# Kernel tuning notes

Measured on AMD Instinct MI355X. Metric: run time of the kernel, lower is better.

The kernel has to match this reference:

```python
import jax, jax.numpy as jnp
import numpy as np

D = 64          # slot_dim == input_dim
K = 8           # num_slots
NUM_ITERS = 3
EPS = 1e-8      # attention renorm eps
LN_EPS = 1e-5   # torch LayerNorm default
SCALE = float(np.sqrt(D))


def _ln(x, g, b):
    m = x.mean(-1, keepdims=True)
    v = ((x - m) ** 2).mean(-1, keepdims=True)
    return (x - m) / jnp.sqrt(v + LN_EPS) * g + b


def setup_inputs() -> dict:
    key = jax.random.key(0)
    ks = jax.random.split(key, 12)
    B, N = 128, 4096
    s = 1.0 / np.sqrt(D)
    return {
        "inputs": jax.random.normal(ks[0], (B, N, D), jnp.float32),
        "noise": jax.random.normal(ks[1], (B, K, D), jnp.float32),
        "slot_mu": jax.random.normal(ks[2], (1, 1, D), jnp.float32),
        "slot_log_sigma": jnp.zeros((1, 1, D), jnp.float32),
        "Wq": jax.random.normal(ks[3], (D, D), jnp.float32) * s,
        "Wk": jax.random.normal(ks[4], (D, D), jnp.float32) * s,
        "Wv": jax.random.normal(ks[5], (D, D), jnp.float32) * s,
        "gru_wih": jax.random.normal(ks[6], (3 * D, D), jnp.float32) * s,
        "gru_whh": jax.random.normal(ks[7], (3 * D, D), jnp.float32) * s,
        "gru_bih": jnp.zeros((3 * D,), jnp.float32),
        "gru_bhh": jnp.zeros((3 * D,), jnp.float32),
        "ln_in_g": jnp.ones((D,), jnp.float32),
        "ln_in_b": jnp.zeros((D,), jnp.float32),
        "ln_s_g": jnp.ones((D,), jnp.float32),
        "ln_s_b": jnp.zeros((D,), jnp.float32),
        "mlp_ln_g": jnp.ones((D,), jnp.float32),
        "mlp_ln_b": jnp.zeros((D,), jnp.float32),
        "mlp_w1": jax.random.normal(ks[8], (4 * D, D), jnp.float32) * s,
        "mlp_b1": jnp.zeros((4 * D,), jnp.float32),
        "mlp_w2": jax.random.normal(ks[9], (D, 4 * D), jnp.float32) * (1.0 / np.sqrt(4 * D)),
        "mlp_b2": jnp.zeros((D,), jnp.float32),
    }


def reference(inputs, noise, slot_mu, slot_log_sigma, Wq, Wk, Wv,
              gru_wih, gru_whh, gru_bih, gru_bhh,
              ln_in_g, ln_in_b, ln_s_g, ln_s_b,
              mlp_ln_g, mlp_ln_b, mlp_w1, mlp_b1, mlp_w2, mlp_b2):
    x = _ln(inputs, ln_in_g, ln_in_b)          # (B, N, D)
    k = x @ Wk.T                               # (B, N, D)
    v = x @ Wv.T                               # (B, N, D)
    slots = slot_mu + jnp.exp(slot_log_sigma) * noise  # (B, K, D)
    for _ in range(NUM_ITERS):
        slots_prev = slots
        s = _ln(slots, ln_s_g, ln_s_b)
        q = s @ Wq.T                           # (B, K, D)
        attn = jnp.einsum('bkd,bnd->bkn', q, k) / SCALE
        attn = jax.nn.softmax(attn, axis=1)    # compete over slots
        attn_w = attn / (attn.sum(-1, keepdims=True) + EPS)
        updates = jnp.einsum('bkn,bnd->bkd', attn_w, v)
        # GRUCell(updates, slots_prev)
        gi = updates @ gru_wih.T + gru_bih
        gh = slots_prev @ gru_whh.T + gru_bhh
        i_r, i_z, i_n = jnp.split(gi, 3, axis=-1)
        h_r, h_z, h_n = jnp.split(gh, 3, axis=-1)
        r = jax.nn.sigmoid(i_r + h_r)
        z = jax.nn.sigmoid(i_z + h_z)
        n = jnp.tanh(i_n + r * h_n)
        slots = (1.0 - z) * n + z * slots_prev
        # residual MLP
        h = _ln(slots, mlp_ln_g, mlp_ln_b)
        slots = slots + jax.nn.relu(h @ mlp_w1.T + mlp_b1) @ mlp_w2.T + mlp_b2
    return slots
```

## Files before the change

kernel.cpp:

```cpp
#include <hip/hip_runtime.h>
#include <cstdint>

#define Bn 128
#define Nn 4096
#define Dn 64
#define Kn 8
#define PBn 8
#define NCHUNKn (Nn / PBn)
#define LN_EPSf 1e-5f
#define EPSf 1e-8f

typedef unsigned short u16x8 __attribute__((ext_vector_type(8)));

static __device__ __forceinline__ uint16_t f2bf(float f) {
    union { float f; uint32_t u; } v; v.f = f;
    return (uint16_t)((v.u + 0x7fffu + ((v.u >> 16) & 1u)) >> 16);
}
static __device__ __forceinline__ float bflo(uint32_t u) {
    union { uint32_t u; float f; } v; v.u = u << 16; return v.f;
}
static __device__ __forceinline__ float bfhi(uint32_t u) {
    union { uint32_t u; float f; } v; v.u = u & 0xffff0000u; return v.f;
}

template <int CTRL>
static __device__ __forceinline__ float dppadd(float x) {
    int p = __builtin_amdgcn_update_dpp(0, __float_as_int(x), CTRL, 0xf, 0xf, false);
    return x + __int_as_float(p);
}

__global__ __launch_bounds__(256) void kinit(const float* __restrict__ noise,
                                             const float* __restrict__ mu,
                                             const float* __restrict__ ls,
                                             float* __restrict__ slots) {
    int i = blockIdx.x * 256 + threadIdx.x;
    int base = i * 4;
    int d = base & 63;
    float4 nz = *(const float4*)(noise + base);
    float4 m  = *(const float4*)(mu + d);
    float4 s  = *(const float4*)(ls + d);
    float4 o;
    o.x = m.x + __expf(s.x) * nz.x;
    o.y = m.y + __expf(s.y) * nz.y;
    o.z = m.z + __expf(s.z) * nz.z;
    o.w = m.w + __expf(s.w) * nz.w;
    *(float4*)(slots + base) = o;
}

__global__ __launch_bounds__(256) void kM(const float* __restrict__ Wq,
                                          const float* __restrict__ Wk,
                                          float* __restrict__ M) {
    const int idx = blockIdx.x * 256 + threadIdx.x;
    const int e = idx >> 6, f = idx & 63;
    float acc = 0.f;
#pragma unroll 8
    for (int d = 0; d < 64; ++d) acc += Wq[d * 64 + e] * Wk[d * 64 + f];
    M[idx] = acc * 0.125f;
}

__global__ __launch_bounds__(256) void k1_ln(const float* __restrict__ inp,
                                             const float* __restrict__ lng,
                                             const float* __restrict__ lnb,
                                             uint16_t* __restrict__ xout) {
    const int t = threadIdx.x;
    const long row = (long)blockIdx.x * 64 + (t >> 2);
    const int c0 = (t & 3) * 16;

    const float* src = inp + row * 64 + c0;
    float x[16];
#pragma unroll
    for (int u = 0; u < 4; ++u) {
        float4 v4 = *(const float4*)(src + u * 4);
        x[u * 4 + 0] = v4.x; x[u * 4 + 1] = v4.y;
        x[u * 4 + 2] = v4.z; x[u * 4 + 3] = v4.w;
    }
    float s1 = 0.f, s2 = 0.f;
#pragma unroll
    for (int i = 0; i < 16; ++i) { s1 += x[i]; s2 += x[i] * x[i]; }
    s1 = dppadd<0xB1>(s1); s2 = dppadd<0xB1>(s2);
    s1 = dppadd<0x4E>(s1); s2 = dppadd<0x4E>(s2);
    const float mean = s1 * (1.0f / 64.0f);
    const float var = s2 * (1.0f / 64.0f) - mean * mean;
    const float rstd = rsqrtf(var + LN_EPSf);

    u16x8 o0, o1;
#pragma unroll
    for (int i = 0; i < 8; ++i) {
        o0[i] = f2bf((x[i] - mean) * rstd * lng[c0 + i] + lnb[c0 + i]);
        o1[i] = f2bf((x[8 + i] - mean) * rstd * lng[c0 + 8 + i] + lnb[c0 + 8 + i]);
    }
    uint16_t* dst = xout + row * 64 + c0;
    *(u16x8*)dst = o0;
    *(u16x8*)(dst + 8) = o1;
}

__global__ __launch_bounds__(256) void k2_attn(
    const uint16_t* __restrict__ xbf, const float* __restrict__ slots,
    const float* __restrict__ M, const float* __restrict__ lsg,
    const float* __restrict__ lsb, float* __restrict__ partials) {
    __shared__ float sraw[Kn * Dn];
    __shared__ float sln[Kn][68];
    __shared__ float qld[Kn][64];
    __shared__ float red[16 * 552];
    __shared__ float redas[16][8];

    const int t = threadIdx.x;
    const int b = blockIdx.x >> 3;
    const int part = blockIdx.x & 7;

    if (t < 128) *(float4*)(sraw + t * 4) = *(const float4*)(slots + b * 512 + t * 4);
    __syncthreads();

    if (t < 128) {
        const int row = t >> 4, l16 = t & 15;
        float4 v4 = *(const float4*)(sraw + row * 64 + l16 * 4);
        float s1 = v4.x + v4.y + v4.z + v4.w;
        float s2 = v4.x * v4.x + v4.y * v4.y + v4.z * v4.z + v4.w * v4.w;
        s1 = dppadd<0xB1>(s1); s2 = dppadd<0xB1>(s2);
        s1 = dppadd<0x4E>(s1); s2 = dppadd<0x4E>(s2);
        s1 = dppadd<0x141>(s1); s2 = dppadd<0x141>(s2);
        s1 = dppadd<0x128>(s1); s2 = dppadd<0x128>(s2);
        const float mean = s1 * (1.0f / 64.0f);
        const float var = s2 * (1.0f / 64.0f) - mean * mean;
        const float rstd = rsqrtf(var + LN_EPSf);
        const float xs[4] = {v4.x, v4.y, v4.z, v4.w};
#pragma unroll
        for (int i = 0; i < 4; ++i) {
            const int dcol = l16 * 4 + i;
            sln[row][dcol] = (xs[i] - mean) * rstd * lsg[dcol] + lsb[dcol];
        }
    }
    __syncthreads();

    {
        const int kk0 = t >> 6, kk1 = kk0 + 4;
        const int j = t & 63;
        float a0 = 0.f, a1 = 0.f;
#pragma unroll 8
        for (int e = 0; e < 64; ++e) {
            const float m = M[e * 64 + j];
            a0 += sln[kk0][e] * m;
            a1 += sln[kk1][e] * m;
        }
        qld[kk0][j] = a0;
        qld[kk1][j] = a1;
    }
    __syncthreads();

    const int dc = t & 7;
    const int pg = t >> 3;
    float qr[8][8];
#pragma unroll
    for (int kk = 0; kk < 8; ++kk) {
        float4 q0 = *(const float4*)&qld[kk][dc * 8];
        float4 q1 = *(const float4*)&qld[kk][dc * 8 + 4];
        qr[kk][0] = q0.x; qr[kk][1] = q0.y; qr[kk][2] = q0.z; qr[kk][3] = q0.w;
        qr[kk][4] = q1.x; qr[kk][5] = q1.y; qr[kk][6] = q1.z; qr[kk][7] = q1.w;
    }

    float upd[8][8];
    float asum[8];
#pragma unroll
    for (int kk = 0; kk < 8; ++kk) {
        asum[kk] = 0.f;
#pragma unroll
        for (int i = 0; i < 8; ++i) upd[kk][i] = 0.f;
    }

    const uint16_t* xbase = xbf + ((long)b * Nn + part * NCHUNKn) * 64 + dc * 8;

    uint4 xr = *(const uint4*)(xbase + (long)pg * 64);

    for (int it = 0; it < NCHUNKn / 32; ++it) {
        uint4 xn = xr;
        if (it < NCHUNKn / 32 - 1)
            xn = *(const uint4*)(xbase + (long)((it + 1) * 32 + pg) * 64);
        float xf[8];
        xf[0] = bflo(xr.x); xf[1] = bfhi(xr.x);
        xf[2] = bflo(xr.y); xf[3] = bfhi(xr.y);
        xf[4] = bflo(xr.z); xf[5] = bfhi(xr.z);
        xf[6] = bflo(xr.w); xf[7] = bfhi(xr.w);

        float lg[8];
#pragma unroll
        for (int kk = 0; kk < 8; ++kk) {
            float a = 0.f;
#pragma unroll
            for (int i = 0; i < 8; ++i) a += qr[kk][i] * xf[i];
            lg[kk] = a;
        }
#pragma unroll
        for (int kk = 0; kk < 8; ++kk) lg[kk] = dppadd<0xB1>(lg[kk]);
#pragma unroll
        for (int kk = 0; kk < 8; ++kk) lg[kk] = dppadd<0x4E>(lg[kk]);
#pragma unroll
        for (int kk = 0; kk < 8; ++kk) lg[kk] = dppadd<0x141>(lg[kk]);
        float mx = lg[0];
#pragma unroll
        for (int kk = 1; kk < 8; ++kk) mx = fmaxf(mx, lg[kk]);
        float e[8];
        float es = 0.f;
#pragma unroll
        for (int kk = 0; kk < 8; ++kk) { e[kk] = __expf(lg[kk] - mx); es += e[kk]; }
        const float rinv = 1.0f / es;
#pragma unroll
        for (int kk = 0; kk < 8; ++kk) {
            const float a = e[kk] * rinv;
            asum[kk] += a;
#pragma unroll
            for (int i = 0; i < 8; ++i) upd[kk][i] += a * xf[i];
        }
        xr = xn;
    }

#pragma unroll
    for (int kk = 0; kk < 8; ++kk) {
#pragma unroll
        for (int i = 0; i < 8; ++i) upd[kk][i] = dppadd<0x128>(upd[kk][i]);
        asum[kk] = dppadd<0x128>(asum[kk]);
    }
    const int l = t & 63;
    const int wv = t >> 6;
    if ((l & 8) == 0) {
        const int copy = wv * 4 + (l >> 4);
        float* rb = red + copy * 552 + (l & 7) * 8;
#pragma unroll
        for (int kk = 0; kk < 8; ++kk) {
            float4 u0, u1;
            u0.x = upd[kk][0]; u0.y = upd[kk][1]; u0.z = upd[kk][2]; u0.w = upd[kk][3];
            u1.x = upd[kk][4]; u1.y = upd[kk][5]; u1.z = upd[kk][6]; u1.w = upd[kk][7];
            *(float4*)(rb + kk * 68) = u0;
            *(float4*)(rb + kk * 68 + 4) = u1;
        }
        if ((l & 15) == 0) {
            float4 a0, a1;
            a0.x = asum[0]; a0.y = asum[1]; a0.z = asum[2]; a0.w = asum[3];
            a1.x = asum[4]; a1.y = asum[5]; a1.z = asum[6]; a1.w = asum[7];
            *(float4*)&redas[copy][0] = a0;
            *(float4*)&redas[copy][4] = a1;
        }
    }
    __syncthreads();
    float* pout = partials + (long)(b * PBn + part) * 520;
    if (t < 128) {
        const int kk = t >> 4, dq = t & 15;
        float4 acc = {0.f, 0.f, 0.f, 0.f};
#pragma unroll
        for (int c = 0; c < 16; ++c) {
            float4 v = *(const float4*)(red + c * 552 + kk * 68 + dq * 4);
            acc.x += v.x; acc.y += v.y; acc.z += v.z; acc.w += v.w;
        }
        *(float4*)(pout + kk * 64 + dq * 4) = acc;
    }
    if (t < 8) {
        float a = 0.f;
#pragma unroll
        for (int c = 0; c < 16; ++c) a += redas[c][t];
        pout[512 + t] = a;
    }
}

__global__ __launch_bounds__(256) void k3_update(
    const float* __restrict__ partials, const float* __restrict__ slots_in,
    const float* __restrict__ Wv,
    const float* __restrict__ wih, const float* __restrict__ whh,
    const float* __restrict__ bih, const float* __restrict__ bhh,
    const float* __restrict__ mg, const float* __restrict__ mb,
    const float* __restrict__ w1, const float* __restrict__ b1,
    const float* __restrict__ w2, const float* __restrict__ b2,
    float* __restrict__ slots_out) {
    __shared__ float axn[64];
    __shared__ float updf[64];
    __shared__ float sp[64];
    __shared__ float gi[192];
    __shared__ float gh[192];
    __shared__ float sn[64];
    __shared__ float hln[64];
    __shared__ float hid[256];

    const int t = threadIdx.x;
    const int b = blockIdx.x >> 3;
    const int s = blockIdx.x & 7;
    const float* pp = partials + (long)b * PBn * 520;

    float asum = EPSf;
#pragma unroll
    for (int j = 0; j < PBn; ++j) asum += pp[j * 520 + 512 + s];
    const float rasum = 1.0f / asum;

    if (t < 64) {
        float a = 0.f;
#pragma unroll
        for (int j = 0; j < PBn; ++j) a += pp[j * 520 + s * 64 + t];
        axn[t] = a * rasum;
    } else if (t < 80) {
        const int i = t - 64;
        *(float4*)&sp[i * 4] = *(const float4*)(slots_in + b * 512 + s * 64 + i * 4);
    }
    __syncthreads();

    {
        const int d = t >> 2, h = t & 3;
        const float* wr = Wv + d * 64 + h * 16;
        float acc = 0.f;
#pragma unroll
        for (int u = 0; u < 4; ++u) {
            float4 w4 = *(const float4*)(wr + u * 4);
            float4 a4 = *(const float4*)&axn[h * 16 + u * 4];
            acc += w4.x * a4.x + w4.y * a4.y + w4.z * a4.z + w4.w * a4.w;
        }
        acc = dppadd<0xB1>(acc);
        acc = dppadd<0x4E>(acc);
        if (h == 0) updf[d] = acc;
    }
    __syncthreads();

    for (int w = t; w < 768; w += 256) {
        const int j = w >> 2, h = w & 3;
        const float* wr = wih + j * 64 + h * 16;
        float acc = 0.f;
#pragma unroll
        for (int u = 0; u < 4; ++u) {
            float4 w4 = *(const float4*)(wr + u * 4);
            float4 a4 = *(const float4*)&updf[h * 16 + u * 4];
            acc += w4.x * a4.x + w4.y * a4.y + w4.z * a4.z + w4.w * a4.w;
        }
        acc = dppadd<0xB1>(acc);
        acc = dppadd<0x4E>(acc);
        if (h == 0) gi[j] = acc + bih[j];
    }
    for (int w = t; w < 768; w += 256) {
        const int j = w >> 2, h = w & 3;
        const float* wr = whh + j * 64 + h * 16;
        float acc = 0.f;
#pragma unroll
        for (int u = 0; u < 4; ++u) {
            float4 w4 = *(const float4*)(wr + u * 4);
            float4 a4 = *(const float4*)&sp[h * 16 + u * 4];
            acc += w4.x * a4.x + w4.y * a4.y + w4.z * a4.z + w4.w * a4.w;
        }
        acc = dppadd<0xB1>(acc);
        acc = dppadd<0x4E>(acc);
        if (h == 0) gh[j] = acc + bhh[j];
    }
    __syncthreads();

    if (t < 64) {
        const float ir = gi[t], iz = gi[64 + t], in_ = gi[128 + t];
        const float hr = gh[t], hz = gh[64 + t], hn = gh[128 + t];
        const float r = 1.0f / (1.0f + __expf(-(ir + hr)));
        const float z = 1.0f / (1.0f + __expf(-(iz + hz)));
        const float n = tanhf(in_ + r * hn);
        sn[t] = (1.0f - z) * n + z * sp[t];
    }
    __syncthreads();

    if (t < 16) {
        float4 v4 = *(const float4*)&sn[t * 4];
        float s1 = v4.x + v4.y + v4.z + v4.w;
        float s2 = v4.x * v4.x + v4.y * v4.y + v4.z * v4.z + v4.w * v4.w;
        s1 = dppadd<0xB1>(s1); s2 = dppadd<0xB1>(s2);
        s1 = dppadd<0x4E>(s1); s2 = dppadd<0x4E>(s2);
        s1 = dppadd<0x141>(s1); s2 = dppadd<0x141>(s2);
        s1 = dppadd<0x128>(s1); s2 = dppadd<0x128>(s2);
        const float mean = s1 * (1.0f / 64.0f);
        const float var = s2 * (1.0f / 64.0f) - mean * mean;
        const float rstd = rsqrtf(var + LN_EPSf);
        const float xs[4] = {v4.x, v4.y, v4.z, v4.w};
#pragma unroll
        for (int i = 0; i < 4; ++i) {
            const int dcol = t * 4 + i;
            hln[dcol] = (xs[i] - mean) * rstd * mg[dcol] + mb[dcol];
        }
    }
    __syncthreads();

    for (int w = t; w < 1024; w += 256) {
        const int j = w >> 2, h = w & 3;
        const float* wr = w1 + j * 64 + h * 16;
        float acc = 0.f;
#pragma unroll
        for (int u = 0; u < 4; ++u) {
            float4 w4 = *(const float4*)(wr + u * 4);
            float4 a4 = *(const float4*)&hln[h * 16 + u * 4];
            acc += w4.x * a4.x + w4.y * a4.y + w4.z * a4.z + w4.w * a4.w;
        }
        acc = dppadd<0xB1>(acc);
        acc = dppadd<0x4E>(acc);
        if (h == 0) hid[j] = fmaxf(acc + b1[j], 0.0f);
    }
    __syncthreads();

    {
        const int d = t >> 2, h = t & 3;
        const float* wr = w2 + d * 256 + h * 64;
        float acc = 0.f;
#pragma unroll
        for (int u = 0; u < 16; ++u) {
            float4 w4 = *(const float4*)(wr + u * 4);
            float4 h4 = *(const float4*)&hid[h * 64 + u * 4];
            acc += w4.x * h4.x + w4.y * h4.y + w4.z * h4.z + w4.w * h4.w;
        }
        acc = dppadd<0xB1>(acc);
        acc = dppadd<0x4E>(acc);
        if (h == 0) slots_out[(long)b * 512 + s * 64 + d] = sn[d] + acc + b2[d];
    }
}

extern "C" void kernel_launch(void* const* d_in, const int* in_sizes, int n_in,
                              void* d_out, int out_size, void* d_ws, size_t ws_size,
                              hipStream_t stream) {
    const float* inputs = (const float*)d_in[0];
    const float* noise = (const float*)d_in[1];
    const float* mu = (const float*)d_in[2];
    const float* ls = (const float*)d_in[3];
    const float* Wq = (const float*)d_in[4];
    const float* Wk = (const float*)d_in[5];
    const float* Wv = (const float*)d_in[6];
    const float* wih = (const float*)d_in[7];
    const float* whh = (const float*)d_in[8];
    const float* bih = (const float*)d_in[9];
    const float* bhh = (const float*)d_in[10];
    const float* lng = (const float*)d_in[11];
    const float* lnb = (const float*)d_in[12];
    const float* lsg = (const float*)d_in[13];
    const float* lsb = (const float*)d_in[14];
    const float* mg = (const float*)d_in[15];
    const float* mb = (const float*)d_in[16];
    const float* w1 = (const float*)d_in[17];
    const float* b1 = (const float*)d_in[18];
    const float* w2 = (const float*)d_in[19];
    const float* b2 = (const float*)d_in[20];

    char* ws = (char*)d_ws;
    float* slots = (float*)ws;
    float* Mm = (float*)(ws + 262144);
    uint16_t* xbf = (uint16_t*)(ws + 262144 + 16384);
    float* parts = (float*)(ws + 262144 + 16384 + (1 << 26));

    kinit<<<64, 256, 0, stream>>>(noise, mu, ls, slots);
    kM<<<16, 256, 0, stream>>>(Wq, Wk, Mm);
    k1_ln<<<8192, 256, 0, stream>>>(inputs, lng, lnb, xbf);
    for (int it = 0; it < 3; ++it) {
        k2_attn<<<Bn * PBn, 256, 0, stream>>>(xbf, slots, Mm, lsg, lsb, parts);
        float* dst = (it == 2) ? (float*)d_out : slots;
        k3_update<<<Bn * Kn, 256, 0, stream>>>(parts, slots, Wv, wih, whh, bih, bhh,
                                               mg, mb, w1, b1, w2, b2, dst);
    }
}
```

Baseline: 210.4 us.

## Split attention over more blocks and process two tokens per loop iteration

Each batch's token range is now split across 16 blocks instead of 8, which doubles the grid of the attention kernel to raise occupancy. The inner loop is fully unrolled and handles two tokens per iteration with two outstanding loads, adding instruction-level parallelism. The softmax across slots no longer subtracts the running maximum, and it uses a hardware reciprocal instead of a divide, cutting ALU work per token. Dropping the max subtraction risks exp overflow if logits grow large. The larger split also doubles the partial buffers that the later reduction has to combine.

```diff
diff --git a/kernel.cpp b/kernel.cpp
--- a/kernel.cpp
+++ b/kernel.cpp
@@ -5,7 +5,7 @@
 #define Nn 4096
 #define Dn 64
 #define Kn 8
-#define PBn 8
+#define PBn 16
 #define NCHUNKn (Nn / PBn)
 #define LN_EPSf 1e-5f
 #define EPSf 1e-8f
@@ -105,8 +105,8 @@
     __shared__ float redas[16][8];
 
     const int t = threadIdx.x;
-    const int b = blockIdx.x >> 3;
-    const int part = blockIdx.x & 7;
+    const int b = blockIdx.x >> 4;
+    const int part = blockIdx.x & 15;
 
     if (t < 128) *(float4*)(sraw + t * 4) = *(const float4*)(slots + b * 512 + t * 4);
     __syncthreads();
@@ -169,48 +169,63 @@
 
     const uint16_t* xbase = xbf + ((long)b * Nn + part * NCHUNKn) * 64 + dc * 8;
 
-    uint4 xr = *(const uint4*)(xbase + (long)pg * 64);
-
-    for (int it = 0; it < NCHUNKn / 32; ++it) {
-        uint4 xn = xr;
-        if (it < NCHUNKn / 32 - 1)
-            xn = *(const uint4*)(xbase + (long)((it + 1) * 32 + pg) * 64);
-        float xf[8];
-        xf[0] = bflo(xr.x); xf[1] = bfhi(xr.x);
-        xf[2] = bflo(xr.y); xf[3] = bfhi(xr.y);
-        xf[4] = bflo(xr.z); xf[5] = bfhi(xr.z);
-        xf[6] = bflo(xr.w); xf[7] = bfhi(xr.w);
-
-        float lg[8];
+    uint4 xr0 = *(const uint4*)(xbase + (long)pg * 64);
+    uint4 xr1 = *(const uint4*)(xbase + (long)(32 + pg) * 64);
+
+#pragma unroll
+    for (int it = 0; it < NCHUNKn / 64; ++it) {
+        uint4 xn0 = xr0, xn1 = xr1;
+        if (it < NCHUNKn / 64 - 1) {
+            xn0 = *(const uint4*)(xbase + (long)((it + 1) * 64 + pg) * 64);
+            xn1 = *(const uint4*)(xbase + (long)((it + 1) * 64 + 32 + pg) * 64);
+        }
+        float xf0[8], xf1[8];
+        xf0[0] = bflo(xr0.x); xf0[1] = bfhi(xr0.x);
+        xf0[2] = bflo(xr0.y); xf0[3] = bfhi(xr0.y);
+        xf0[4] = bflo(xr0.z); xf0[5] = bfhi(xr0.z);
+        xf0[6] = bflo(xr0.w); xf0[7] = bfhi(xr0.w);
+        xf1[0] = bflo(xr1.x); xf1[1] = bfhi(xr1.x);
+        xf1[2] = bflo(xr1.y); xf1[3] = bfhi(xr1.y);
+        xf1[4] = bflo(xr1.z); xf1[5] = bfhi(xr1.z);
+        xf1[6] = bflo(xr1.w); xf1[7] = bfhi(xr1.w);
+
+        float lg0[8], lg1[8];
 #pragma unroll
         for (int kk = 0; kk < 8; ++kk) {
-            float a = 0.f;
-#pragma unroll
-            for (int i = 0; i < 8; ++i) a += qr[kk][i] * xf[i];
-            lg[kk] = a;
-        }
-#pragma unroll
-        for (int kk = 0; kk < 8; ++kk) lg[kk] = dppadd<0xB1>(lg[kk]);
-#pragma unroll
-        for (int kk = 0; kk < 8; ++kk) lg[kk] = dppadd<0x4E>(lg[kk]);
-#pragma unroll
-        for (int kk = 0; kk < 8; ++kk) lg[kk] = dppadd<0x141>(lg[kk]);
-        float mx = lg[0];
-#pragma unroll
-        for (int kk = 1; kk < 8; ++kk) mx = fmaxf(mx, lg[kk]);
-        float e[8];
-        float es = 0.f;
-#pragma unroll
-        for (int kk = 0; kk < 8; ++kk) { e[kk] = __expf(lg[kk] - mx); es += e[kk]; }
-        const float rinv = 1.0f / es;
+            float a0 = 0.f, a1 = 0.f;
+#pragma unroll
+            for (int i = 0; i < 8; ++i) {
+                a0 += qr[kk][i] * xf0[i];
+                a1 += qr[kk][i] * xf1[i];
+            }
+            lg0[kk] = a0;
+            lg1[kk] = a1;
+        }
+#pragma unroll
+        for (int kk = 0; kk < 8; ++kk) { lg0[kk] = dppadd<0xB1>(lg0[kk]); lg1[kk] = dppadd<0xB1>(lg1[kk]); }
+#pragma unroll
+        for (int kk = 0; kk < 8; ++kk) { lg0[kk] = dppadd<0x4E>(lg0[kk]); lg1[kk] = dppadd<0x4E>(lg1[kk]); }
+#pragma unroll
+        for (int kk = 0; kk < 8; ++kk) { lg0[kk] = dppadd<0x141>(lg0[kk]); lg1[kk] = dppadd<0x141>(lg1[kk]); }
+        float e0[8], e1[8];
+        float es0 = 0.f, es1 = 0.f;
 #pragma unroll
         for (int kk = 0; kk < 8; ++kk) {
-            const float a = e[kk] * rinv;
-            asum[kk] += a;
-#pragma unroll
-            for (int i = 0; i < 8; ++i) upd[kk][i] += a * xf[i];
-        }
-        xr = xn;
+            e0[kk] = __expf(lg0[kk]); es0 += e0[kk];
+            e1[kk] = __expf(lg1[kk]); es1 += e1[kk];
+        }
+        const float r0 = __builtin_amdgcn_rcpf(es0);
+        const float r1 = __builtin_amdgcn_rcpf(es1);
+#pragma unroll
+        for (int kk = 0; kk < 8; ++kk) {
+            const float a0 = e0[kk] * r0;
+            const float a1 = e1[kk] * r1;
+            asum[kk] += a0 + a1;
+#pragma unroll
+            for (int i = 0; i < 8; ++i)
+                upd[kk][i] += a0 * xf0[i] + a1 * xf1[i];
+        }
+        xr0 = xn0; xr1 = xn1;
     }
 
 #pragma unroll
```

Measured after the change: 282.7 us. 1.34x slower.

## Precompute slot queries in update kernel and simplify attention softmax with exp2

Applied to the files above, without the earlier changes.

Slot LayerNorm and the query projection through M are moved out of the attention kernel. They now run in an init kernel and at the end of the GRU/MLP update kernel, which writes a qk buffer. The attention kernel then only loads precomputed queries, so its 8 blocks per batch no longer each redo that work. The softmax over slots drops the max subtraction, uses exp2 with log2(e) folded into M, and uses a fast reciprocal. This trades numerical safety against overflow for fewer instructions per token. An unused kinit_qk kernel is left behind as dead code.

```diff
diff --git a/kernel.cpp b/kernel.cpp
--- a/kernel.cpp
+++ b/kernel.cpp
@@ -9,6 +9,7 @@
 #define NCHUNKn (Nn / PBn)
 #define LN_EPSf 1e-5f
 #define EPSf 1e-8f
+#define LOG2Ef 1.4426950408889634f
 
 typedef unsigned short u16x8 __attribute__((ext_vector_type(8)));
 
@@ -27,24 +28,6 @@
 static __device__ __forceinline__ float dppadd(float x) {
     int p = __builtin_amdgcn_update_dpp(0, __float_as_int(x), CTRL, 0xf, 0xf, false);
     return x + __int_as_float(p);
-}
-
-__global__ __launch_bounds__(256) void kinit(const float* __restrict__ noise,
-                                             const float* __restrict__ mu,
-                                             const float* __restrict__ ls,
-                                             float* __restrict__ slots) {
-    int i = blockIdx.x * 256 + threadIdx.x;
-    int base = i * 4;
-    int d = base & 63;
-    float4 nz = *(const float4*)(noise + base);
-    float4 m  = *(const float4*)(mu + d);
-    float4 s  = *(const float4*)(ls + d);
-    float4 o;
-    o.x = m.x + __expf(s.x) * nz.x;
-    o.y = m.y + __expf(s.y) * nz.y;
-    o.z = m.z + __expf(s.z) * nz.z;
-    o.w = m.w + __expf(s.w) * nz.w;
-    *(float4*)(slots + base) = o;
 }
 
 __global__ __launch_bounds__(256) void kM(const float* __restrict__ Wq,
@@ -55,62 +38,33 @@
     float acc = 0.f;
 #pragma unroll 8
     for (int d = 0; d < 64; ++d) acc += Wq[d * 64 + e] * Wk[d * 64 + f];
-    M[idx] = acc * 0.125f;
-}
-
-__global__ __launch_bounds__(256) void k1_ln(const float* __restrict__ inp,
-                                             const float* __restrict__ lng,
-                                             const float* __restrict__ lnb,
-                                             uint16_t* __restrict__ xout) {
-    const int t = threadIdx.x;
-    const long row = (long)blockIdx.x * 64 + (t >> 2);
-    const int c0 = (t & 3) * 16;
-
-    const float* src = inp + row * 64 + c0;
-    float x[16];
-#pragma unroll
-    for (int u = 0; u < 4; ++u) {
-        float4 v4 = *(const float4*)(src + u * 4);
-        x[u * 4 + 0] = v4.x; x[u * 4 + 1] = v4.y;
-        x[u * 4 + 2] = v4.z; x[u * 4 + 3] = v4.w;
-    }
-    float s1 = 0.f, s2 = 0.f;
-#pragma unroll
-    for (int i = 0; i < 16; ++i) { s1 += x[i]; s2 += x[i] * x[i]; }
-    s1 = dppadd<0xB1>(s1); s2 = dppadd<0xB1>(s2);
-    s1 = dppadd<0x4E>(s1); s2 = dppadd<0x4E>(s2);
-    const float mean = s1 * (1.0f / 64.0f);
-    const float var = s2 * (1.0f / 64.0f) - mean * mean;
-    const float rstd = rsqrtf(var + LN_EPSf);
-
-    u16x8 o0, o1;
-#pragma unroll
-    for (int i = 0; i < 8; ++i) {
-        o0[i] = f2bf((x[i] - mean) * rstd * lng[c0 + i] + lnb[c0 + i]);
-        o1[i] = f2bf((x[8 + i] - mean) * rstd * lng[c0 + 8 + i] + lnb[c0 + 8 + i]);
-    }
-    uint16_t* dst = xout + row * 64 + c0;
-    *(u16x8*)dst = o0;
-    *(u16x8*)(dst + 8) = o1;
-}
-
-__global__ __launch_bounds__(256) void k2_attn(
-    const uint16_t* __restrict__ xbf, const float* __restrict__ slots,
-    const float* __restrict__ M, const float* __restrict__ lsg,
-    const float* __restrict__ lsb, float* __restrict__ partials) {
+    M[idx] = acc * 0.125f * LOG2Ef;
+}
+
+__global__ __launch_bounds__(256) void kinit_qk(
+    const float* __restrict__ noise, const float* __restrict__ mu,
+    const float* __restrict__ ls, const float* __restrict__ M,
+    float* __restrict__ slots, float* __restrict__ qk) {
     __shared__ float sraw[Kn * Dn];
     __shared__ float sln[Kn][68];
-    __shared__ float qld[Kn][64];
-    __shared__ float red[16 * 552];
-    __shared__ float redas[16][8];
-
     const int t = threadIdx.x;
-    const int b = blockIdx.x >> 3;
-    const int part = blockIdx.x & 7;
-
-    if (t < 128) *(float4*)(sraw + t * 4) = *(const float4*)(slots + b * 512 + t * 4);
-    __syncthreads();
-
+    const int b = blockIdx.x;
+
+    if (t < 128) {
+        const int base = (b * 128 + t) * 4;
+        const int d = base & 63;
+        float4 nz = *(const float4*)(noise + base);
+        float4 m4 = *(const float4*)(mu + d);
+        float4 s4 = *(const float4*)(ls + d);
+        float4 o;
+        o.x = m4.x + __expf(s4.x) * nz.x;
+        o.y = m4.y + __expf(s4.y) * nz.y;
+        o.z = m4.z + __expf(s4.z) * nz.z;
+        o.w = m4.w + __expf(s4.w) * nz.w;
+        *(float4*)(slots + base) = o;
+        *(float4*)(sraw + t * 4) = o;
+    }
+    __syncthreads();
     if (t < 128) {
         const int row = t >> 4, l16 = t & 15;
         float4 v4 = *(const float4*)(sraw + row * 64 + l16 * 4);
@@ -125,26 +79,114 @@
         const float rstd = rsqrtf(var + LN_EPSf);
         const float xs[4] = {v4.x, v4.y, v4.z, v4.w};
 #pragma unroll
+        for (int i = 0; i < 4; ++i) sln[row][l16 * 4 + i] = (xs[i] - mean) * rstd;
+    }
+    __syncthreads();
+    ((void)0);
+}
+
+__global__ __launch_bounds__(256) void kinit_qk_full(
+    const float* __restrict__ noise, const float* __restrict__ mu,
+    const float* __restrict__ ls, const float* __restrict__ M,
+    const float* __restrict__ lsg, const float* __restrict__ lsb,
+    float* __restrict__ slots, float* __restrict__ qk) {
+    __shared__ float sraw[Kn * Dn];
+    __shared__ float sln[Kn][68];
+    const int t = threadIdx.x;
+    const int b = blockIdx.x;
+
+    if (t < 128) {
+        const int base = (b * 128 + t) * 4;
+        const int d = base & 63;
+        float4 nz = *(const float4*)(noise + base);
+        float4 m4 = *(const float4*)(mu + d);
+        float4 s4 = *(const float4*)(ls + d);
+        float4 o;
+        o.x = m4.x + __expf(s4.x) * nz.x;
+        o.y = m4.y + __expf(s4.y) * nz.y;
+        o.z = m4.z + __expf(s4.z) * nz.z;
+        o.w = m4.w + __expf(s4.w) * nz.w;
+        *(float4*)(slots + base) = o;
+        *(float4*)(sraw + t * 4) = o;
+    }
+    __syncthreads();
+    if (t < 128) {
+        const int row = t >> 4, l16 = t & 15;
+        float4 v4 = *(const float4*)(sraw + row * 64 + l16 * 4);
+        float s1 = v4.x + v4.y + v4.z + v4.w;
+        float s2 = v4.x * v4.x + v4.y * v4.y + v4.z * v4.z + v4.w * v4.w;
+        s1 = dppadd<0xB1>(s1); s2 = dppadd<0xB1>(s2);
+        s1 = dppadd<0x4E>(s1); s2 = dppadd<0x4E>(s2);
+        s1 = dppadd<0x141>(s1); s2 = dppadd<0x141>(s2);
+        s1 = dppadd<0x128>(s1); s2 = dppadd<0x128>(s2);
+        const float mean = s1 * (1.0f / 64.0f);
+        const float var = s2 * (1.0f / 64.0f) - mean * mean;
+        const float rstd = rsqrtf(var + LN_EPSf);
+        const float xs[4] = {v4.x, v4.y, v4.z, v4.w};
+#pragma unroll
         for (int i = 0; i < 4; ++i) {
             const int dcol = l16 * 4 + i;
             sln[row][dcol] = (xs[i] - mean) * rstd * lsg[dcol] + lsb[dcol];
         }
     }
     __syncthreads();
-
-    {
-        const int kk0 = t >> 6, kk1 = kk0 + 4;
-        const int j = t & 63;
-        float a0 = 0.f, a1 = 0.f;
+    for (int o = t; o < 512; o += 256) {
+        const int kk = o >> 6, j = o & 63;
+        float a = 0.f;
 #pragma unroll 8
-        for (int e = 0; e < 64; ++e) {
-            const float m = M[e * 64 + j];
-            a0 += sln[kk0][e] * m;
-            a1 += sln[kk1][e] * m;
-        }
-        qld[kk0][j] = a0;
-        qld[kk1][j] = a1;
-    }
+        for (int e = 0; e < 64; ++e) a += sln[kk][e] * M[e * 64 + j];
+        qk[b * 512 + o] = a;
+    }
+}
+
+__global__ __launch_bounds__(256) void k1_ln(const float* __restrict__ inp,
+                                             const float* __restrict__ lng,
+                                             const float* __restrict__ lnb,
+                                             uint16_t* __restrict__ xout) {
+    const int t = threadIdx.x;
+    const long row = (long)blockIdx.x * 64 + (t >> 2);
+    const int c0 = (t & 3) * 16;
+
+    const float* src = inp + row * 64 + c0;
+    float x[16];
+#pragma unroll
+    for (int u = 0; u < 4; ++u) {
+        float4 v4 = *(const float4*)(src + u * 4);
+        x[u * 4 + 0] = v4.x; x[u * 4 + 1] = v4.y;
+        x[u * 4 + 2] = v4.z; x[u * 4 + 3] = v4.w;
+    }
+    float s1 = 0.f, s2 = 0.f;
+#pragma unroll
+    for (int i = 0; i < 16; ++i) { s1 += x[i]; s2 += x[i] * x[i]; }
+    s1 = dppadd<0xB1>(s1); s2 = dppadd<0xB1>(s2);
+    s1 = dppadd<0x4E>(s1); s2 = dppadd<0x4E>(s2);
+    const float mean = s1 * (1.0f / 64.0f);
+    const float var = s2 * (1.0f / 64.0f) - mean * mean;
+    const float rstd = rsqrtf(var + LN_EPSf);
+
+    u16x8 o0, o1;
+#pragma unroll
+    for (int i = 0; i < 8; ++i) {
+        o0[i] = f2bf((x[i] - mean) * rstd * lng[c0 + i] + lnb[c0 + i]);
+        o1[i] = f2bf((x[8 + i] - mean) * rstd * lng[c0 + 8 + i] + lnb[c0 + 8 + i]);
+    }
+    uint16_t* dst = xout + row * 64 + c0;
+    *(u16x8*)dst = o0;
+    *(u16x8*)(dst + 8) = o1;
+}
+
+__global__ __launch_bounds__(256) void k2_attn(
+    const uint16_t* __restrict__ xbf, const float* __restrict__ qkg,
+    float* __restrict__ partials) {
+    __shared__ float qld[Kn][64];
+    __shared__ float red[16 * 552];
+    __shared__ float redas[16][8];
+
+    const int t = threadIdx.x;
+    const int b = blockIdx.x >> 3;
+    const int part = blockIdx.x & 7;
+
+    if (t < 128) *(float4*)(&qld[0][0] + t * 4) = *(const float4*)(qkg + b * 512 + t * 4);
     __syncthreads();
 
     const int dc = t & 7;
@@ -195,14 +237,11 @@
         for (int kk = 0; kk < 8; ++kk) lg[kk] = dppadd<0x4E>(lg[kk]);
 #pragma unroll
         for (int kk = 0; kk < 8; ++kk) lg[kk] = dppadd<0x141>(lg[kk]);
-        float mx = lg[0];
-#pragma unroll
-        for (int kk = 1; kk < 8; ++kk) mx = fmaxf(mx, lg[kk]);
         float e[8];
         float es = 0.f;
 #pragma unroll
-        for (int kk = 0; kk < 8; ++kk) { e[kk] = __expf(lg[kk] - mx); es += e[kk]; }
-        const float rinv = 1.0f / es;
+        for (int kk = 0; kk < 8; ++kk) { e[kk] = exp2f(lg[kk]); es += e[kk]; }
+        const float rinv = __builtin_amdgcn_rcpf(es);
 #pragma unroll
         for (int kk = 0; kk < 8; ++kk) {
             const float a = e[kk] * rinv;
@@ -268,7 +307,9 @@
     const float* __restrict__ mg, const float* __restrict__ mb,
     const float* __restrict__ w1, const float* __restrict__ b1,
     const float* __restrict__ w2, const float* __restrict__ b2,
-    float* __restrict__ slots_out) {
+    const float* __restrict__ M, const float* __restrict__ lsg,
+    const float* __restrict__ lsb,
+    float* __restrict__ slots_out, float* __restrict__ qkout) {
     __shared__ float axn[64];
     __shared__ float updf[64];
     __shared__ float sp[64];
@@ -277,6 +318,8 @@
     __shared__ float sn[64];
     __shared__ float hln[64];
     __shared__ float hid[256];
+    __shared__ float outv[64];
+    __shared__ float lnq[64];
 
     const int t = threadIdx.x;
     const int b = blockIdx.x >> 3;
@@ -403,7 +446,38 @@
         }
         acc = dppadd<0xB1>(acc);
         acc = dppadd<0x4E>(acc);
-        if (h == 0) slots_out[(long)b * 512 + s * 64 + d] = sn[d] + acc + b2[d];
+        if (h == 0) {
+            const float val = sn[d] + acc + b2[d];
+            slots_out[(long)b * 512 + s * 64 + d] = val;
+            outv[d] = val;
+        }
+    }
+    __syncthreads();
+
+    if (t < 16) {
+        float4 v4 = *(const float4*)&outv[t * 4];
+        float s1 = v4.x + v4.y + v4.z + v4.w;
+        float s2 = v4.x * v4.x + v4.y * v4.y + v4.z * v4.z + v4.w * v4.w;
+        s1 = dppadd<0xB1>(s1); s2 = dppadd<0xB1>(s2);
+        s1 = dppadd<0x4E>(s1); s2 = dppadd<0x4E>(s2);
+        s1 = dppadd<0x141>(s1); s2 = dppadd<0x141>(s2);
+        s1 = dppadd<0x128>(s1); s2 = dppadd<0x128>(s2);
+        const float mean = s1 * (1.0f / 64.0f);
+        const float var = s2 * (1.0f / 64.0f) - mean * mean;
+        const float rstd = rsqrtf(var + LN_EPSf);
+        const float xs[4] = {v4.x, v4.y, v4.z, v4.w};
+#pragma unroll
+        for (int i = 0; i < 4; ++i) {
+            const int dcol = t * 4 + i;
+            lnq[dcol] = (xs[i] - mean) * rstd * lsg[dcol] + lsb[dcol];
+        }
+    }
+    __syncthreads();
+    if (t < 64) {
+        float a = 0.f;
+#pragma unroll 8
+        for (int e = 0; e < 64; ++e) a += lnq[e] * M[e * 64 + t];
+        qkout[b * 512 + s * 64 + t] = a;
     }
 }
 
@@ -435,16 +509,18 @@
     char* ws = (char*)d_ws;
     float* slots = (float*)ws;
     float* Mm = (float*)(ws + 262144);
-    uint16_t* xbf = (uint16_t*)(ws + 262144 + 16384);
-    float* parts = (float*)(ws + 262144 + 16384 + (1 << 26));
-
-    kinit<<<64, 256, 0, stream>>>(noise, mu, ls, slots);
+    float* qk = (float*)(ws + 262144 + 16384);
+    uint16_t* xbf = (uint16_t*)(ws + 262144 + 16384 + 262144);
+    float* parts = (float*)(ws + 262144 + 16384 + 262144 + (1 << 26));
+
     kM<<<16, 256, 0, stream>>>(Wq, Wk, Mm);
+    kinit_qk_full<<<Bn, 256, 0, stream>>>(noise, mu, ls, Mm, lsg, lsb, slots, qk);
     k1_ln<<<8192, 256, 0, stream>>>(inputs, lng, lnb, xbf);
     for (int it = 0; it < 3; ++it) {
-        k2_attn<<<Bn * PBn, 256, 0, stream>>>(xbf, slots, Mm, lsg, lsb, parts);
+        k2_attn<<<Bn * PBn, 256, 0, stream>>>(xbf, qk, parts);
         float* dst = (it == 2) ? (float*)d_out : slots;
         k3_update<<<Bn * Kn, 256, 0, stream>>>(parts, slots, Wv, wih, whh, bih, bhh,
-                                               mg, mb, w1, b1, w2, b2, dst);
-    }
-}
+                                               mg, mb, w1, b1, w2, b2, Mm, lsg, lsb,
+                                               dst, qk);
+    }
+}
```

New measurement: 202.1 us. 1.04x faster.
